# Optimization experiments

Hardware: AMD Instinct MI355X
Metric: run time of the kernel (lower is better)

The kernel has to match this reference:

```python
import jax, jax.numpy as jnp
import numpy as np

# model dims (DeepSeekV2-Lite-like, reduced expert count)
H = 2048      # hidden_dim
NH = 16       # num_heads
NOPE = 128    # qk_nope_head_dim
ROPE = 64     # qk_rope_head_dim (interleaved rotary)
VD = 128      # v_head_dim
QL = 1536     # q_lora_rank
KVL = 512     # kv_lora_rank
E = 8         # num routed experts
TOPK = 2      # num_experts_per_token
MI = 512      # moe_intermediate_dim
SH_I = 2 * MI # num_shared_experts * moe_intermediate_dim
B = 1
S = 2048
T = B * S
EPS = 1e-6
MOE_SCALE = 1.0  # gating_scaling_factor


def setup_inputs() -> dict:
    key = jax.random.key(0)
    ks = jax.random.split(key, 16)
    def w(k, shape):
        return jax.random.normal(k, shape, dtype=jnp.float32) * 0.02
    # interleaved rotary tables: one angle per (even,odd) pair
    half = ROPE // 2
    pos = jnp.arange(S, dtype=jnp.float32)
    inv_freq = 1.0 / (10000.0 ** (jnp.arange(half, dtype=jnp.float32) * 2.0 / ROPE))
    ang = pos[:, None] * inv_freq[None, :]              # [S, half]
    sin = jnp.tile(jnp.sin(ang), (B, 1))                # [T, half]
    cos = jnp.tile(jnp.cos(ang), (B, 1))
    return {
        "x": jax.random.normal(ks[0], (T, H), jnp.float32),
        "skip": jax.random.normal(ks[1], (T, H), jnp.float32),
        "rotary_sin": sin,
        "rotary_cos": cos,
        "ln1_w": jnp.ones((H,), jnp.float32),
        "ln2_w": jnp.ones((H,), jnp.float32),
        "w_qa": w(ks[2], (QL, H)),
        "qa_norm_w": jnp.ones((QL,), jnp.float32),
        "w_qb": w(ks[3], (NH * (NOPE + ROPE), QL)),
        "w_kva": w(ks[4], (KVL + ROPE, H)),
        "kva_norm_w": jnp.ones((KVL,), jnp.float32),
        "w_kb": w(ks[5], (NH * NOPE, KVL)),
        "w_vb": w(ks[6], (NH * VD, KVL)),
        "w_o": w(ks[7], (H, NH * VD)),
        "gate_w": w(ks[8], (E, H)),
        "moe_up_w": w(ks[9], (E, 2 * MI, H)),
        "moe_down_w": w(ks[10], (E, H, MI)),
        "shared_up_w": w(ks[11], (2 * SH_I, H)),
        "shared_down_w": w(ks[12], (H, SH_I)),
        "batch": B,
    }


def _rms(v, w):
    return v * jax.lax.rsqrt(jnp.mean(v * v, axis=-1, keepdims=True) + EPS) * w


def _rope_interleaved(v, sin, cos):
    # v: [T, nh, ROPE]; sin/cos: [T, ROPE//2]; rotate (even, odd) pairs
    x1, x2 = v[..., 0::2], v[..., 1::2]
    s, c = sin[:, None, :], cos[:, None, :]
    o1 = x1 * c - x2 * s
    o2 = x1 * s + x2 * c
    return jnp.stack([o1, o2], axis=-1).reshape(v.shape)


def reference(x, skip, rotary_sin, rotary_cos, ln1_w, ln2_w, w_qa, qa_norm_w,
              w_qb, w_kva, kva_norm_w, w_kb, w_vb, w_o, gate_w,
              moe_up_w, moe_down_w, shared_up_w, shared_down_w, batch):
    Tt = x.shape[0]
    Sq = Tt // batch
    # SkipRMSNorm #1
    x1 = x + skip
    n1 = _rms(x1, ln1_w)
    # ---- MLA attention (prefill path, decoding_batches=0) ----
    qa = _rms(n1 @ w_qa.T, qa_norm_w)                               # [T, QL]
    q = (qa @ w_qb.T).reshape(Tt, NH, NOPE + ROPE)
    q_nope, q_pe = q[..., :NOPE], q[..., NOPE:]
    q_pe = _rope_interleaved(q_pe, rotary_sin, rotary_cos)
    kv = n1 @ w_kva.T                                               # [T, KVL+ROPE]
    ckv = _rms(kv[:, :KVL], kva_norm_w)
    k_pe = _rope_interleaved(kv[:, KVL:][:, None, :], rotary_sin, rotary_cos)  # [T,1,ROPE]
    k_nope = (ckv @ w_kb.T).reshape(Tt, NH, NOPE)
    v = (ckv @ w_vb.T).reshape(Tt, NH, VD)
    qf = jnp.concatenate([q_nope, q_pe], -1).reshape(batch, Sq, NH, NOPE + ROPE)
    kf = jnp.concatenate([k_nope, jnp.broadcast_to(k_pe, (Tt, NH, ROPE))], -1)
    kf = kf.reshape(batch, Sq, NH, NOPE + ROPE)
    vf = v.reshape(batch, Sq, NH, VD)
    scale = 1.0 / np.sqrt(NOPE + ROPE)
    scores = jnp.einsum('bqhd,bkhd->bhqk', qf, kf) * scale
    causal = jnp.tril(jnp.ones((Sq, Sq), bool))
    scores = jnp.where(causal[None, None], scores, jnp.float32(-1e30))
    p = jax.nn.softmax(scores, axis=-1)
    o = jnp.einsum('bhqk,bkhd->bqhd', p, vf).reshape(Tt, NH * VD)
    attn = o @ w_o.T
    # SkipRMSNorm #2
    x2 = x1 + attn
    n2 = _rms(x2, ln2_w)
    # ---- MoE FFN: softmax gate, greedy top-k, normalized probs ----
    probs = jax.nn.softmax(n2 @ gate_w.T, axis=-1)                  # [T, E]
    tv, ti = jax.lax.top_k(probs, TOPK)
    tv = tv / jnp.sum(tv, axis=-1, keepdims=True) * MOE_SCALE
    routed = jnp.zeros_like(n2)
    for e in range(E):  # fixed small expert count; masked dense dispatch
        we = jnp.sum(tv * (ti == e), axis=-1)                       # [T]
        h = n2 @ moe_up_w[e].T                                      # [T, 2*MI]
        h = jax.nn.silu(h[:, :MI]) * h[:, MI:]
        routed = routed + we[:, None] * (h @ moe_down_w[e].T)
    # shared experts (dense swiglu MLP)
    hs = n2 @ shared_up_w.T
    hs = jax.nn.silu(hs[:, :SH_I]) * hs[:, SH_I:]
    ffn = routed + hs @ shared_down_w.T
    return (x2, ffn)
```

## Files before the change

kernel.cpp:

```cpp
#include <hip/hip_runtime.h>
#include <hip/hip_bf16.h>

#define H 2048
#define NH 16
#define NOPE 128
#define ROPE_D 64
#define DQK 192
#define VD 128
#define QL 1536
#define KVL 512
#define NE 8
#define MI_D 512
#define SHI 1024
#define EPS 1e-6f
#define MAXA 5120

typedef unsigned short bfu;
typedef short bf16x8 __attribute__((ext_vector_type(8)));
typedef float f32x4 __attribute__((ext_vector_type(4)));

#define MFMA16(a, b, c) __builtin_amdgcn_mfma_f32_16x16x32_bf16(a, b, c, 0, 0, 0)

#define BAR_PLAIN()   asm volatile("s_barrier" ::: "memory")
#define BAR_LGKM0()   asm volatile("s_waitcnt lgkmcnt(0)\n\ts_barrier" ::: "memory")
#define BAR_VM4()     asm volatile("s_waitcnt vmcnt(4)\n\ts_barrier" ::: "memory")
#define BAR_VM0()     asm volatile("s_waitcnt vmcnt(0)\n\ts_barrier" ::: "memory")

__device__ __forceinline__ float bf2f(bfu u) {
    union { unsigned int i; float f; } w; w.i = ((unsigned int)u) << 16; return w.f;
}
__device__ __forceinline__ bfu f2bf(float f) {
    union { float f; unsigned int i; } u; u.f = f;
    return (bfu)((u.i + 0x7fffu + ((u.i >> 16) & 1u)) >> 16);
}

__device__ __forceinline__ void async16(const bfu* g, bfu* l) {
    __builtin_amdgcn_global_load_lds((const __attribute__((address_space(1))) void*)g,
                                     (__attribute__((address_space(3))) void*)l, 16, 0, 0);
}

__device__ __forceinline__ float blk_sum(float v) {
    __shared__ float sb[4];
    for (int o = 32; o > 0; o >>= 1) v += __shfl_down(v, o, 64);
    int lane = threadIdx.x & 63, w = threadIdx.x >> 6;
    __syncthreads();
    if (lane == 0) sb[w] = v;
    __syncthreads();
    return sb[0] + sb[1] + sb[2] + sb[3];
}

struct GemmSeg {
    const bfu* A; const bfu* B; void* C; void* C2;
    const int* aidx; const int* eid;
    long bstride;
    int N, K, ldm3, mode, nx, ntiles;
};

__device__ __forceinline__ void gemm_body(const bfu* __restrict__ A, const bfu* __restrict__ B,
                                          void* __restrict__ Cv, void* __restrict__ Cv2,
                                          int N, int K, int ldm3, int mode,
                                          const int* __restrict__ aidx,
                                          const int* __restrict__ eid, long bstride,
                                          int bx, int by,
                                          bfu* sAb, bfu* sBb) {
    bfu (*sA)[128 * 32] = (bfu (*)[128 * 32])sAb;
    bfu (*sB)[128 * 32] = (bfu (*)[128 * 32])sBb;
    const int tid = threadIdx.x;
    const int lane = tid & 63, w = tid >> 6;
    const int quad = lane >> 4, li = lane & 15;
    const int m0 = by * 128, n0 = bx * 128;
    const bfu* Bp = B + (eid ? (size_t)eid[by] * bstride : 0);

    const int l4 = lane >> 2;
    const int lg = lane & 3;
    const int kc = lg ^ ((lane >> 3) & 3);
    int r0 = m0 + w * 32 + l4, r1 = r0 + 16;
    if (aidx) { r0 = aidx[r0]; r1 = aidx[r1]; }
    const bfu* gA0 = A + (size_t)r0 * K + kc * 8;
    const bfu* gA1 = A + (size_t)r1 * K + kc * 8;
    const bfu* gB0 = Bp + (size_t)(n0 + w * 32 + l4) * K + kc * 8;
    const bfu* gB1 = gB0 + (size_t)16 * K;
    const int oA0 = (w * 32) * 32, oA1 = (w * 32 + 16) * 32;

    const int wm = (w >> 1) * 64, wn = (w & 1) * 64;
    const int fg = (quad ^ ((li >> 1) & 3)) * 8;
    int oa[4], ob[4];
#pragma unroll
    for (int t4 = 0; t4 < 4; ++t4) {
        oa[t4] = (wm + t4 * 16 + li) * 32 + fg;
        ob[t4] = (wn + t4 * 16 + li) * 32 + fg;
    }
    f32x4 acc[4][4];
#pragma unroll
    for (int i = 0; i < 4; ++i)
#pragma unroll
        for (int j = 0; j < 4; ++j) acc[i][j] = (f32x4){0.f, 0.f, 0.f, 0.f};

    const int nb = K / 32;
    async16(gA0, &sA[0][oA0]); async16(gA1, &sA[0][oA1]);
    async16(gB0, &sB[0][oA0]); async16(gB1, &sB[0][oA1]);
    async16(gA0 + 32, &sA[1][oA0]); async16(gA1 + 32, &sA[1][oA1]);
    async16(gB0 + 32, &sB[1][oA0]); async16(gB1 + 32, &sB[1][oA1]);

    int cur = 0;
    for (int it = 0; it < nb; ++it) {
        if (it < nb - 1) { BAR_VM4(); } else { BAR_VM0(); }
        bf16x8 av[4], bv[4];
#pragma unroll
        for (int t4 = 0; t4 < 4; ++t4) av[t4] = *(const bf16x8*)&sA[cur][oa[t4]];
#pragma unroll
        for (int t4 = 0; t4 < 4; ++t4) bv[t4] = *(const bf16x8*)&sB[cur][ob[t4]];
        if (it + 2 < nb) {
            const int k1 = (it + 2) * 32;
            int nxt = cur + 2; if (nxt >= 3) nxt -= 3;
            async16(gA0 + k1, &sA[nxt][oA0]); async16(gA1 + k1, &sA[nxt][oA1]);
            async16(gB0 + k1, &sB[nxt][oA0]); async16(gB1 + k1, &sB[nxt][oA1]);
        }
#pragma unroll
        for (int mt = 0; mt < 4; ++mt)
#pragma unroll
            for (int nt = 0; nt < 4; ++nt)
                acc[mt][nt] = MFMA16(av[mt], bv[nt], acc[mt][nt]);
        if (++cur >= 3) cur = 0;
    }

#pragma unroll
    for (int mt = 0; mt < 4; ++mt)
#pragma unroll
        for (int nt = 0; nt < 4; ++nt) {
            int row = m0 + wm + mt * 16 + quad * 4;
            int col = n0 + wn + nt * 16 + li;
            if (mode == 0) {
                float* C = (float*)Cv;
#pragma unroll
                for (int r = 0; r < 4; ++r) C[(size_t)(row + r) * N + col] = acc[mt][nt][r];
            } else if (mode == 1) {
                bfu* C = (bfu*)Cv;
#pragma unroll
                for (int r = 0; r < 4; ++r) C[(size_t)(row + r) * N + col] = f2bf(acc[mt][nt][r]);
            } else {
                if (n0 < 2048) {
                    bfu* C = (bfu*)Cv;
#pragma unroll
                    for (int r = 0; r < 4; ++r) C[(size_t)(row + r) * 2048 + col] = f2bf(acc[mt][nt][r]);
                } else {
                    bfu* C2 = (bfu*)Cv2;
                    ushort4 u;
                    u.x = f2bf(acc[mt][nt][0]); u.y = f2bf(acc[mt][nt][1]);
                    u.z = f2bf(acc[mt][nt][2]); u.w = f2bf(acc[mt][nt][3]);
                    *(ushort4*)(C2 + (size_t)(col - 2048) * ldm3 + row) = u;
                }
            }
        }
}

__global__ __launch_bounds__(256) void gemm_multi(GemmSeg s0, GemmSeg s1) {
    __shared__ bfu sA[3][128 * 32];
    __shared__ bfu sB[3][128 * 32];
    int b = blockIdx.x;
    if (b < s0.ntiles) {
        gemm_body(s0.A, s0.B, s0.C, s0.C2, s0.N, s0.K, s0.ldm3, s0.mode,
                  s0.aidx, s0.eid, s0.bstride, b % s0.nx, b / s0.nx, &sA[0][0], &sB[0][0]);
    } else {
        int lb = b - s0.ntiles;
        gemm_body(s1.A, s1.B, s1.C, s1.C2, s1.N, s1.K, s1.ldm3, s1.mode,
                  s1.aidx, s1.eid, s1.bstride, lb % s1.nx, lb / s1.nx, &sA[0][0], &sB[0][0]);
    }
}

struct CastArgs {
    const float* s[10];
    bfu* d[10];
    unsigned start[11];
    int pad[10];
};
__global__ __launch_bounds__(256) void k_cast_all(CastArgs a) {
    unsigned g = blockIdx.x * 256 + threadIdx.x;
    if (g >= a.start[10]) return;
    int id = 0;
#pragma unroll
    for (int i = 1; i < 10; ++i) if (g >= a.start[i]) id = i;
    size_t i16 = (size_t)(g - a.start[id]) * 16;
    ushort4 u[4] = {};
    if (!a.pad[id] || (i16 >> 11) < 576) {
        const float* s = a.s[id];
#pragma unroll
        for (int j = 0; j < 4; ++j) {
            float4 x = *(const float4*)(s + i16 + j * 4);
            u[j].x = f2bf(x.x); u[j].y = f2bf(x.y); u[j].z = f2bf(x.z); u[j].w = f2bf(x.w);
        }
    }
    bfu* d = a.d[id];
#pragma unroll
    for (int j = 0; j < 4; ++j) *(ushort4*)(d + i16 + j * 4) = u[j];
}

__global__ __launch_bounds__(256) void k_add_rms(const float* __restrict__ x, const float* __restrict__ skip,
                                                 const float* __restrict__ w,
                                                 float* __restrict__ x1, bfu* __restrict__ n1b) {
    int t = blockIdx.x;
    size_t base = (size_t)t * H;
    float loc[8]; float ss = 0.f;
#pragma unroll
    for (int i = 0; i < 8; ++i) {
        int c = threadIdx.x + i * 256;
        float v = x[base + c] + skip[base + c];
        loc[i] = v; ss += v * v;
        x1[base + c] = v;
    }
    float tot = blk_sum(ss);
    float r = rsqrtf(tot / (float)H + EPS);
#pragma unroll
    for (int i = 0; i < 8; ++i) {
        int c = threadIdx.x + i * 256;
        n1b[base + c] = f2bf(loc[i] * r * w[c]);
    }
}

__global__ __launch_bounds__(256) void k_qkv_post(const bfu* __restrict__ qkv,
                                                  const float* __restrict__ qa_nw,
                                                  const float* __restrict__ kva_nw,
                                                  const float* __restrict__ sin_, const float* __restrict__ cos_,
                                                  bfu* __restrict__ qab, bfu* __restrict__ ckv,
                                                  bfu* __restrict__ kpe) {
    int t = blockIdx.x;
    const bfu* row = qkv + (size_t)t * 2176;
    float qa[6]; float ss1 = 0.f;
#pragma unroll
    for (int i = 0; i < 6; ++i) {
        float v = bf2f(row[threadIdx.x + i * 256]); qa[i] = v; ss1 += v * v;
    }
    float v0 = bf2f(row[1536 + threadIdx.x]), v1 = bf2f(row[1792 + threadIdx.x]);
    float s1 = blk_sum(ss1);
    float s2 = blk_sum(v0 * v0 + v1 * v1);
    float r1 = rsqrtf(s1 / (float)QL + EPS);
    float r2 = rsqrtf(s2 / 512.f + EPS);
#pragma unroll
    for (int i = 0; i < 6; ++i) {
        int c = threadIdx.x + i * 256;
        qab[(size_t)t * QL + c] = f2bf(qa[i] * r1 * qa_nw[c]);
    }
    ckv[(size_t)t * 512 + threadIdx.x]       = f2bf(v0 * r2 * kva_nw[threadIdx.x]);
    ckv[(size_t)t * 512 + threadIdx.x + 256] = f2bf(v1 * r2 * kva_nw[threadIdx.x + 256]);
    if (threadIdx.x < 32) {
        int p = threadIdx.x;
        float x1v = bf2f(row[2048 + 2 * p]), x2v = bf2f(row[2048 + 2 * p + 1]);
        float s = sin_[t * 32 + p], c = cos_[t * 32 + p];
        kpe[(size_t)t * 64 + 2 * p]     = f2bf(x1v * c - x2v * s);
        kpe[(size_t)t * 64 + 2 * p + 1] = f2bf(x1v * s + x2v * c);
    }
}

__global__ __launch_bounds__(256) void k_flash_mfma(const bfu* __restrict__ qb,
                                                    const bfu* __restrict__ kn,
                                                    const bfu* __restrict__ kpe,
                                                    const bfu* __restrict__ vt,
                                                    bfu* __restrict__ O,
                                                    const float* __restrict__ rsin,
                                                    const float* __restrict__ rcos, int T) {
    __shared__ bfu Ks[64 * 200];
    __shared__ bfu VtL[2][128 * 32];
    __shared__ bfu P[64 * 72];
    const int tid = threadIdx.x;
    const int lane = tid & 63, w = tid >> 6;
    const int quad = lane >> 4, li = lane & 15;
    const int q0 = ((int)gridDim.x - 1 - (int)blockIdx.x) * 64;
    const int h = blockIdx.y;
    const float scale = 0.07216878364870322f;

    bf16x8 qf[6];
    {
        int qrow = q0 + w * 16 + li;
        const bfu* qp = qb + ((size_t)qrow * NH + h) * DQK;
#pragma unroll
        for (int s6 = 0; s6 < 6; ++s6) {
            bf16x8 v = *(const bf16x8*)(qp + s6 * 32 + quad * 8);
            if (s6 >= 4) {
                int pb = (s6 - 4) * 16 + quad * 4;
#pragma unroll
                for (int j = 0; j < 4; ++j) {
                    float x1 = bf2f((bfu)v[2 * j]), x2 = bf2f((bfu)v[2 * j + 1]);
                    float s = rsin[qrow * 32 + pb + j], c = rcos[qrow * 32 + pb + j];
                    v[2 * j]     = (short)f2bf(x1 * c - x2 * s);
                    v[2 * j + 1] = (short)f2bf(x1 * s + x2 * c);
                }
            }
            qf[s6] = v;
        }
    }
    f32x4 accO[8];
#pragma unroll
    for (int i = 0; i < 8; ++i) accO[i] = (f32x4){0.f, 0.f, 0.f, 0.f};
    float lrow[4] = {0.f, 0.f, 0.f, 0.f};

    int kr[6], kg[6];
#pragma unroll
    for (int it = 0; it < 6; ++it) { int G = tid + it * 256; kr[it] = G / 24; kg[it] = G % 24; }
    int vn[4], vgl[4], vkc[4];
#pragma unroll
    for (int it = 0; it < 4; ++it) {
        int idx = tid + it * 256; vn[it] = idx >> 3; vgl[it] = idx & 7;
        vkc[it] = (vgl[it] & 4) | ((vgl[it] & 3) ^ ((vn[it] >> 1) & 3));
    }
    bf16x8 kreg[6], vreg[4];
#pragma unroll
    for (int it = 0; it < 6; ++it)
        kreg[it] = (kg[it] < 16) ? *(const bf16x8*)(kn + (size_t)kr[it] * (NH * 128) + h * 128 + kg[it] * 8)
                                 : *(const bf16x8*)(kpe + (size_t)kr[it] * 64 + (kg[it] - 16) * 8);
#pragma unroll
    for (int it = 0; it < 4; ++it)
        vreg[it] = *(const bf16x8*)(vt + (size_t)(h * 128 + vn[it]) * T + vkc[it] * 8);

    const int fgv = (quad ^ ((li >> 1) & 3)) * 8;
    const int kend = q0 + 64;
    for (int k0 = 0; k0 < kend; k0 += 64) {
        BAR_PLAIN();
#pragma unroll
        for (int it = 0; it < 6; ++it) *(bf16x8*)(Ks + kr[it] * 200 + kg[it] * 8) = kreg[it];
#pragma unroll
        for (int it = 0; it < 4; ++it)
            *(bf16x8*)(VtL[vgl[it] >> 2] + vn[it] * 32 + (vgl[it] & 3) * 8) = vreg[it];
        if (k0 + 64 < kend) {
            int k1 = k0 + 64;
#pragma unroll
            for (int it = 0; it < 6; ++it)
                kreg[it] = (kg[it] < 16) ? *(const bf16x8*)(kn + (size_t)(k1 + kr[it]) * (NH * 128) + h * 128 + kg[it] * 8)
                                         : *(const bf16x8*)(kpe + (size_t)(k1 + kr[it]) * 64 + (kg[it] - 16) * 8);
#pragma unroll
            for (int it = 0; it < 4; ++it)
                vreg[it] = *(const bf16x8*)(vt + (size_t)(h * 128 + vn[it]) * T + k1 + vkc[it] * 8);
        }
        BAR_LGKM0();
        f32x4 s[4];
#pragma unroll
        for (int ct = 0; ct < 4; ++ct) {
            f32x4 a = (f32x4){0.f, 0.f, 0.f, 0.f};
#pragma unroll
            for (int s6 = 0; s6 < 6; ++s6) {
                bf16x8 kf = *(const bf16x8*)(Ks + (ct * 16 + li) * 200 + s6 * 32 + quad * 8);
                a = MFMA16(qf[s6], kf, a);
            }
            s[ct] = a;
        }
#pragma unroll
        for (int ct = 0; ct < 4; ++ct)
#pragma unroll
            for (int r = 0; r < 4; ++r) {
                int row = q0 + w * 16 + quad * 4 + r;
                float p = (k0 + ct * 16 + li <= row) ? __expf(s[ct][r] * scale) : 0.f;
                s[ct][r] = p;
                lrow[r] += p;
            }
#pragma unroll
        for (int ct = 0; ct < 4; ++ct)
#pragma unroll
            for (int r = 0; r < 4; ++r)
                P[(w * 16 + quad * 4 + r) * 72 + ct * 16 + li] = f2bf(s[ct][r]);
        bf16x8 pf[2];
#pragma unroll
        for (int ks = 0; ks < 2; ++ks)
            pf[ks] = *(const bf16x8*)(P + (w * 16 + li) * 72 + ks * 32 + quad * 8);
#pragma unroll
        for (int v8 = 0; v8 < 8; ++v8)
#pragma unroll
            for (int ks = 0; ks < 2; ++ks) {
                bf16x8 vf = *(const bf16x8*)(VtL[ks] + (v8 * 16 + li) * 32 + fgv);
                accO[v8] = MFMA16(pf[ks], vf, accO[v8]);
            }
    }
#pragma unroll
    for (int r = 0; r < 4; ++r) {
        float l = lrow[r];
        l += __shfl_xor(l, 1); l += __shfl_xor(l, 2);
        l += __shfl_xor(l, 4); l += __shfl_xor(l, 8);
        lrow[r] = 1.0f / l;
    }
#pragma unroll
    for (int v8 = 0; v8 < 8; ++v8)
#pragma unroll
        for (int r = 0; r < 4; ++r) {
            float val = accO[v8][r] * lrow[r];
            O[(size_t)(q0 + w * 16 + quad * 4 + r) * (NH * 128) + h * 128 + v8 * 16 + li] = f2bf(val);
        }
}

__global__ __launch_bounds__(256) void k_x2_n2(const float* __restrict__ x1, const bfu* __restrict__ attn,
                                               const float* __restrict__ ln2w, float* __restrict__ outx2,
                                               bfu* __restrict__ n2b, const float* __restrict__ gw,
                                               int* __restrict__ eidx, float* __restrict__ wts,
                                               int* __restrict__ cnt) {
    int t = blockIdx.x;
    size_t base = (size_t)t * H;
    float loc[8]; float ss = 0.f;
#pragma unroll
    for (int i = 0; i < 8; ++i) {
        int c = threadIdx.x + i * 256;
        float vv = x1[base + c] + bf2f(attn[base + c]);
        loc[i] = vv; ss += vv * vv;
        outx2[base + c] = vv;
    }
    float tot = blk_sum(ss);
    float r = rsqrtf(tot / (float)H + EPS);
    float pe[NE] = {0.f, 0.f, 0.f, 0.f, 0.f, 0.f, 0.f, 0.f};
#pragma unroll
    for (int i = 0; i < 8; ++i) {
        int c = threadIdx.x + i * 256;
        float nv = loc[i] * r * ln2w[c];
        n2b[base + c] = f2bf(nv);
#pragma unroll
        for (int e = 0; e < NE; ++e) pe[e] += nv * gw[e * H + c];
    }
    __shared__ float sred[4][NE];
    int lane = threadIdx.x & 63, wv = threadIdx.x >> 6;
#pragma unroll
    for (int e = 0; e < NE; ++e) {
        float v = pe[e];
        for (int o = 32; o > 0; o >>= 1) v += __shfl_down(v, o, 64);
        if (lane == 0) sred[wv][e] = v;
    }
    __syncthreads();
    if (threadIdx.x == 0) {
        float logits[NE];
        float m = -1e30f;
        for (int e = 0; e < NE; ++e) {
            logits[e] = sred[0][e] + sred[1][e] + sred[2][e] + sred[3][e];
            m = fmaxf(m, logits[e]);
        }
        float p[NE];
        for (int e = 0; e < NE; ++e) p[e] = __expf(logits[e] - m);
        int i1 = 0;
        for (int e = 1; e < NE; ++e) if (p[e] > p[i1]) i1 = e;
        int i2 = -1;
        for (int e = 0; e < NE; ++e) if (e != i1 && (i2 < 0 || p[e] > p[i2])) i2 = e;
        float denom = p[i1] + p[i2];
        eidx[t * 2] = i1; eidx[t * 2 + 1] = i2;
        wts[t * 2] = p[i1] / denom; wts[t * 2 + 1] = p[i2] / denom;
        atomicAdd(&cnt[i1], 1); atomicAdd(&cnt[i2], 1);
    }
}

__global__ __launch_bounds__(256) void k_moe_init(int* __restrict__ cnt, int* __restrict__ slot,
                                                  int* __restrict__ eid, int* __restrict__ idx,
                                                  float* __restrict__ aw) {
    int tid = threadIdx.x;
    if (tid < NE) { cnt[tid] = 0; slot[tid] = 0; }
    if (tid < 40) eid[tid] = 0;
    for (int i = tid; i < MAXA; i += 256) { idx[i] = 0; aw[i] = 0.f; }
}

__global__ __launch_bounds__(64) void k_moe_scan(const int* __restrict__ cnt, int* __restrict__ base,
                                                 int* __restrict__ eid) {
    if (threadIdx.x == 0) {
        int off = 0;
        for (int e = 0; e < NE; ++e) {
            base[e] = off;
            int nb = (cnt[e] + 127) >> 7;
            for (int j = 0; j < nb; ++j) eid[(off >> 7) + j] = e;
            off += nb << 7;
        }
    }
}

__global__ __launch_bounds__(256) void k_moe_scatter(const int* __restrict__ eidx, const float* __restrict__ wts,
                                                     const int* __restrict__ base, int* __restrict__ slot,
                                                     int* __restrict__ idx, float* __restrict__ aw,
                                                     int* __restrict__ posmap) {
    int t = blockIdx.x * 256 + threadIdx.x;
#pragma unroll
    for (int j = 0; j < 2; ++j) {
        int e = eidx[t * 2 + j];
        int p = base[e] + atomicAdd(&slot[e], 1);
        idx[p] = t; aw[p] = wts[t * 2 + j]; posmap[t * 2 + j] = p;
    }
}

__global__ __launch_bounds__(256) void k_silu_both(const bfu* __restrict__ hsh, bfu* __restrict__ gsh,
                                                   const bfu* __restrict__ hsp, const float* __restrict__ aw,
                                                   bfu* __restrict__ gsp, int T) {
    int b = blockIdx.x;
    if (b < T) {
        const bfu* row = hsh + (size_t)b * 2048;
        bfu* grow = gsh + (size_t)b * 1024;
#pragma unroll
        for (int j = 0; j < 4; ++j) {
            int i = threadIdx.x + j * 256;
            float a = bf2f(row[i]), bb = bf2f(row[1024 + i]);
            grow[i] = f2bf(a / (1.0f + __expf(-a)) * bb);
        }
    } else {
        int row = b - T;
        float we = aw[row];
        const bfu* hr = hsp + (size_t)row * 1024;
        bfu* gr = gsp + (size_t)row * 512;
#pragma unroll
        for (int j = 0; j < 2; ++j) {
            int i = threadIdx.x + j * 256;
            float a = bf2f(hr[i]), bb = bf2f(hr[512 + i]);
            gr[i] = f2bf(we * a / (1.0f + __expf(-a)) * bb);
        }
    }
}

__global__ __launch_bounds__(256) void k_ffn_out(const float* __restrict__ routed, const bfu* __restrict__ dsp,
                                                 const int* __restrict__ posmap, float* __restrict__ out,
                                                 size_t TH) {
    int t = blockIdx.x;
    int p1 = posmap[t * 2], p2 = posmap[t * 2 + 1];
    const bfu* d1 = dsp + (size_t)p1 * H;
    const bfu* d2 = dsp + (size_t)p2 * H;
#pragma unroll
    for (int j = 0; j < 8; ++j) {
        int c = threadIdx.x + j * 256;
        out[TH + (size_t)t * H + c] = routed[(size_t)t * H + c] + bf2f(d1[c]) + bf2f(d2[c]);
    }
}

static inline GemmSeg mk_seg(const bfu* A, const bfu* B, void* C, void* C2,
                             const int* aidx, const int* eid, long bstride,
                             int N, int K, int ldm3, int mode, int nx, int ny) {
    GemmSeg s;
    s.A = A; s.B = B; s.C = C; s.C2 = C2; s.aidx = aidx; s.eid = eid; s.bstride = bstride;
    s.N = N; s.K = K; s.ldm3 = ldm3; s.mode = mode; s.nx = nx; s.ntiles = nx * ny;
    return s;
}

extern "C" void kernel_launch(void* const* d_in, const int* in_sizes, int n_in,
                              void* d_out, int out_size, void* d_ws, size_t ws_size,
                              hipStream_t stream) {
    const float* x      = (const float*)d_in[0];
    const float* skip   = (const float*)d_in[1];
    const float* rsin   = (const float*)d_in[2];
    const float* rcos   = (const float*)d_in[3];
    const float* ln1w   = (const float*)d_in[4];
    const float* ln2w   = (const float*)d_in[5];
    const float* w_qa   = (const float*)d_in[6];
    const float* qa_nw  = (const float*)d_in[7];
    const float* w_qb   = (const float*)d_in[8];
    const float* w_kva  = (const float*)d_in[9];
    const float* kva_nw = (const float*)d_in[10];
    const float* w_kb   = (const float*)d_in[11];
    const float* w_vb   = (const float*)d_in[12];
    const float* w_o    = (const float*)d_in[13];
    const float* gate_w = (const float*)d_in[14];
    const float* mup    = (const float*)d_in[15];
    const float* mdown  = (const float*)d_in[16];
    const float* shup   = (const float*)d_in[17];
    const float* shdown = (const float*)d_in[18];

    const int T = in_sizes[0] / H;

    bfu* WB = (bfu*)d_ws;
    bfu* wqkv_b  = WB + 0;
    bfu* wkbv_b  = WB + 4456448;
    bfu* wqb_b   = WB + 6553600;
    bfu* wo_b    = WB + 11272192;
    bfu* mup_b   = WB + 15466496;
    bfu* mdown_b = WB + 32243712;
    bfu* shup_b  = WB + 40632320;
    bfu* shdn_b  = WB + 44826624;
    const size_t WBYTES = 93847552;

    char* AB = (char*)d_ws + WBYTES;
    float* x1f    = (float*)(AB + 0);
    float* routed = (float*)(AB + 0);
    bfu*   n1b    = (bfu*)(AB + 16777216);
    bfu*   qkvb   = (bfu*)(AB + 25165824);
    bfu*   knb    = (bfu*)(AB + 25165824);
    bfu*   hsp    = (bfu*)(AB + 25165824);
    bfu*   qab    = (bfu*)(AB + 35651584);
    bfu*   gsp    = (bfu*)(AB + 35651584);
    bfu*   qbb    = (bfu*)(AB + 41943040);
    bfu*   attnb  = (bfu*)(AB + 41943040);
    bfu*   ckvb   = (bfu*)(AB + 54525952);
    bfu*   kpeb   = (bfu*)(AB + 56623104);
    char*  G      = AB + 56885248;
    int*   eidx   = (int*)(G);
    float* wts    = (float*)(G + 16384);
    int*   posmap = (int*)(G + 32768);
    int*   midx   = (int*)(G + 49152);
    float* maw    = (float*)(G + 69632);
    int*   mcnt   = (int*)(G + 90112);
    int*   mbase  = (int*)(G + 90112 + 64);
    int*   mslot  = (int*)(G + 90112 + 128);
    int*   meid   = (int*)(G + 90112 + 192);
    bfu*   ob     = (bfu*)(AB + 57016320);
    bfu*   gsb    = (bfu*)(AB + 57016320);
    bfu*   vtb    = (bfu*)(AB + 65404928);
    bfu*   hsb    = (bfu*)(AB + 65404928);
    bfu*   dsp    = (bfu*)(AB + 65404928);
    const size_t REQ = WBYTES + 86376448;
    if (ws_size < REQ) return;

    {
        CastArgs ca;
        const float* ss[10] = {w_qa, w_kva, w_kb, w_vb, w_qb, w_o, mup, mdown, shup, shdown};
        bfu* dd[10] = {wqkv_b, wqkv_b + 3145728, wkbv_b, wkbv_b + 1048576, wqb_b,
                       wo_b, mup_b, mdown_b, shup_b, shdn_b};
        unsigned n16[10] = {196608, 81920, 65536, 65536, 294912, 262144, 1048576, 524288, 262144, 131072};
        unsigned acc = 0;
        for (int i = 0; i < 10; ++i) { ca.s[i] = ss[i]; ca.d[i] = dd[i]; ca.start[i] = acc; acc += n16[i]; ca.pad[i] = (i == 1); }
        ca.start[10] = acc;
        k_cast_all<<<(acc + 255) / 256, 256, 0, stream>>>(ca);
    }

    k_add_rms<<<T, 256, 0, stream>>>(x, skip, ln1w, x1f, n1b);
    {
        GemmSeg s = mk_seg(n1b, wqkv_b, qkvb, nullptr, nullptr, nullptr, 0, 2176, H, 0, 1, 2176 / 128, T / 128);
        gemm_multi<<<s.ntiles, 256, 0, stream>>>(s, s);
    }
    k_qkv_post<<<T, 256, 0, stream>>>(qkvb, qa_nw, kva_nw, rsin, rcos, qab, ckvb, kpeb);
    {
        GemmSeg sq = mk_seg(qab, wqb_b, qbb, nullptr, nullptr, nullptr, 0, NH * DQK, QL, 0, 1, (NH * DQK) / 128, T / 128);
        GemmSeg sk = mk_seg(ckvb, wkbv_b, knb, vtb, nullptr, nullptr, 0, 4096, KVL, T, 4, 4096 / 128, T / 128);
        gemm_multi<<<sq.ntiles + sk.ntiles, 256, 0, stream>>>(sq, sk);
    }
    k_flash_mfma<<<dim3(T / 64, NH), 256, 0, stream>>>(qbb, knb, kpeb, vtb, ob, rsin, rcos, T);
    {
        GemmSeg s = mk_seg(ob, wo_b, attnb, nullptr, nullptr, nullptr, 0, H, NH * VD, 0, 1, H / 128, T / 128);
        gemm_multi<<<s.ntiles, 256, 0, stream>>>(s, s);
    }
    k_moe_init<<<1, 256, 0, stream>>>(mcnt, mslot, meid, midx, maw);
    k_x2_n2<<<T, 256, 0, stream>>>(x1f, attnb, ln2w, (float*)d_out, n1b, gate_w, eidx, wts, mcnt);
    k_moe_scan<<<1, 64, 0, stream>>>(mcnt, mbase, meid);
    k_moe_scatter<<<T / 256, 256, 0, stream>>>(eidx, wts, mbase, mslot, midx, maw, posmap);
    {
        GemmSeg ssh = mk_seg(n1b, shup_b, hsb, nullptr, nullptr, nullptr, 0, 2048, H, 0, 1, 2048 / 128, T / 128);
        GemmSeg smo = mk_seg(n1b, mup_b, hsp, nullptr, midx, meid, (long)1024 * H, 1024, H, 0, 1, 1024 / 128, MAXA / 128);
        gemm_multi<<<ssh.ntiles + smo.ntiles, 256, 0, stream>>>(ssh, smo);
    }
    k_silu_both<<<T + MAXA, 256, 0, stream>>>(hsb, gsb, hsp, maw, gsp, T);
    {
        GemmSeg ssd = mk_seg(gsb, shdn_b, routed, nullptr, nullptr, nullptr, 0, H, SHI, 0, 0, H / 128, T / 128);
        GemmSeg smd = mk_seg(gsp, mdown_b, dsp, nullptr, nullptr, meid, (long)H * MI_D, H, MI_D, 0, 1, H / 128, MAXA / 128);
        gemm_multi<<<ssd.ntiles + smd.ntiles, 256, 0, stream>>>(ssd, smd);
    }
    k_ffn_out<<<T, 256, 0, stream>>>(routed, dsp, posmap, (float*)d_out, (size_t)T * H);
}
```

Measured before the change: 638.0 us.

## Split weight casts across GEMM launches to overlap conversion with compute

The single up-front fp32-to-bf16 weight cast kernel is removed. Its work is split into four groups, and each group is appended as extra blocks to an earlier gemm_multi launch, so every weight is converted just before the GEMM that needs it. This lets the memory-bound cast run alongside compute-bound GEMM tiles. In exchange, the gemm_multi kernel now carries a large CastArgs struct and a third branch, and the cast blocks share the LDS allocation size of the GEMM blocks, which may limit how many of them stay resident at once.

```diff
diff --git a/kernel.cpp b/kernel.cpp
--- a/kernel.cpp
+++ b/kernel.cpp
@@ -54,6 +54,13 @@
     const int* aidx; const int* eid;
     long bstride;
     int N, K, ldm3, mode, nx, ntiles;
+};
+
+struct CastArgs {
+    const float* s[10];
+    bfu* d[10];
+    unsigned start[11];
+    int pad[10];
 };
 
 __device__ __forceinline__ void gemm_body(const bfu* __restrict__ A, const bfu* __restrict__ B,
@@ -154,45 +161,37 @@
         }
 }
 
-__global__ __launch_bounds__(256) void gemm_multi(GemmSeg s0, GemmSeg s1) {
+__global__ __launch_bounds__(256) void gemm_multi(GemmSeg s0, GemmSeg s1, CastArgs ca) {
     __shared__ bfu sA[3][128 * 32];
     __shared__ bfu sB[3][128 * 32];
     int b = blockIdx.x;
     if (b < s0.ntiles) {
         gemm_body(s0.A, s0.B, s0.C, s0.C2, s0.N, s0.K, s0.ldm3, s0.mode,
                   s0.aidx, s0.eid, s0.bstride, b % s0.nx, b / s0.nx, &sA[0][0], &sB[0][0]);
-    } else {
+    } else if (b < s0.ntiles + s1.ntiles) {
         int lb = b - s0.ntiles;
         gemm_body(s1.A, s1.B, s1.C, s1.C2, s1.N, s1.K, s1.ldm3, s1.mode,
                   s1.aidx, s1.eid, s1.bstride, lb % s1.nx, lb / s1.nx, &sA[0][0], &sB[0][0]);
-    }
-}
-
-struct CastArgs {
-    const float* s[10];
-    bfu* d[10];
-    unsigned start[11];
-    int pad[10];
-};
-__global__ __launch_bounds__(256) void k_cast_all(CastArgs a) {
-    unsigned g = blockIdx.x * 256 + threadIdx.x;
-    if (g >= a.start[10]) return;
-    int id = 0;
-#pragma unroll
-    for (int i = 1; i < 10; ++i) if (g >= a.start[i]) id = i;
-    size_t i16 = (size_t)(g - a.start[id]) * 16;
-    ushort4 u[4] = {};
-    if (!a.pad[id] || (i16 >> 11) < 576) {
-        const float* s = a.s[id];
-#pragma unroll
-        for (int j = 0; j < 4; ++j) {
-            float4 x = *(const float4*)(s + i16 + j * 4);
-            u[j].x = f2bf(x.x); u[j].y = f2bf(x.y); u[j].z = f2bf(x.z); u[j].w = f2bf(x.w);
-        }
-    }
-    bfu* d = a.d[id];
-#pragma unroll
-    for (int j = 0; j < 4; ++j) *(ushort4*)(d + i16 + j * 4) = u[j];
+    } else {
+        unsigned g = (unsigned)(b - s0.ntiles - s1.ntiles) * 256 + threadIdx.x;
+        if (g >= ca.start[10]) return;
+        int id = 0;
+#pragma unroll
+        for (int i = 1; i < 10; ++i) if (g >= ca.start[i]) id = i;
+        size_t i16 = (size_t)(g - ca.start[id]) * 16;
+        ushort4 u[4] = {};
+        if (!ca.pad[id] || (i16 >> 11) < 576) {
+            const float* s = ca.s[id];
+#pragma unroll
+            for (int j = 0; j < 4; ++j) {
+                float4 xv = *(const float4*)(s + i16 + j * 4);
+                u[j].x = f2bf(xv.x); u[j].y = f2bf(xv.y); u[j].z = f2bf(xv.z); u[j].w = f2bf(xv.w);
+            }
+        }
+        bfu* d = ca.d[id];
+#pragma unroll
+        for (int j = 0; j < 4; ++j) *(ushort4*)(d + i16 + j * 4) = u[j];
+    }
 }
 
 __global__ __launch_bounds__(256) void k_add_rms(const float* __restrict__ x, const float* __restrict__ skip,
@@ -522,6 +521,21 @@
     s.A = A; s.B = B; s.C = C; s.C2 = C2; s.aidx = aidx; s.eid = eid; s.bstride = bstride;
     s.N = N; s.K = K; s.ldm3 = ldm3; s.mode = mode; s.nx = nx; s.ntiles = nx * ny;
     return s;
+}
+
+static inline CastArgs mk_cast(int n, const float* const ss[], bfu* const dd[],
+                               const unsigned nn[], const int pp[]) {
+    CastArgs ca;
+    unsigned acc = 0;
+    for (int i = 0; i < n; ++i) {
+        ca.s[i] = ss[i]; ca.d[i] = dd[i]; ca.pad[i] = pp[i];
+        ca.start[i] = acc; acc += nn[i];
+    }
+    for (int i = n; i < 10; ++i) {
+        ca.s[i] = ss[n - 1]; ca.d[i] = dd[n - 1]; ca.pad[i] = 0; ca.start[i] = acc;
+    }
+    ca.start[10] = acc;
+    return ca;
 }
 
 extern "C" void kernel_launch(void* const* d_in, const int* in_sizes, int n_in,
@@ -591,33 +605,54 @@
     const size_t REQ = WBYTES + 86376448;
     if (ws_size < REQ) return;
 
-    {
-        CastArgs ca;
-        const float* ss[10] = {w_qa, w_kva, w_kb, w_vb, w_qb, w_o, mup, mdown, shup, shdown};
-        bfu* dd[10] = {wqkv_b, wqkv_b + 3145728, wkbv_b, wkbv_b + 1048576, wqb_b,
-                       wo_b, mup_b, mdown_b, shup_b, shdn_b};
-        unsigned n16[10] = {196608, 81920, 65536, 65536, 294912, 262144, 1048576, 524288, 262144, 131072};
-        unsigned acc = 0;
-        for (int i = 0; i < 10; ++i) { ca.s[i] = ss[i]; ca.d[i] = dd[i]; ca.start[i] = acc; acc += n16[i]; ca.pad[i] = (i == 1); }
-        ca.start[10] = acc;
-        k_cast_all<<<(acc + 255) / 256, 256, 0, stream>>>(ca);
-    }
-
+    GemmSeg z; z.A = nullptr; z.B = nullptr; z.C = nullptr; z.C2 = nullptr;
+    z.aidx = nullptr; z.eid = nullptr; z.bstride = 0;
+    z.N = 0; z.K = 32; z.ldm3 = 0; z.mode = 1; z.nx = 1; z.ntiles = 0;
+
+    const float* c0s[2] = {w_qa, w_kva};
+    bfu*         c0d[2] = {wqkv_b, wqkv_b + 3145728};
+    unsigned     c0n[2] = {196608, 81920};
+    int          c0p[2] = {0, 1};
+    CastArgs ca0 = mk_cast(2, c0s, c0d, c0n, c0p);
+
+    const float* cQs[3] = {w_qb, w_kb, w_vb};
+    bfu*         cQd[3] = {wqb_b, wkbv_b, wkbv_b + 1048576};
+    unsigned     cQn[3] = {294912, 65536, 65536};
+    int          cQp[3] = {0, 0, 0};
+    CastArgs caQ = mk_cast(3, cQs, cQd, cQn, cQp);
+
+    const float* cBs[2] = {w_o, mup};
+    bfu*         cBd[2] = {wo_b, mup_b};
+    unsigned     cBn[2] = {262144, 1048576};
+    int          cBp[2] = {0, 0};
+    CastArgs caB = mk_cast(2, cBs, cBd, cBn, cBp);
+
+    const float* cWs[3] = {shup, mdown, shdown};
+    bfu*         cWd[3] = {shup_b, mdown_b, shdn_b};
+    unsigned     cWn[3] = {262144, 524288, 131072};
+    int          cWp[3] = {0, 0, 0};
+    CastArgs caW = mk_cast(3, cWs, cWd, cWn, cWp);
+
+    const float* cEs[1] = {w_qa}; bfu* cEd[1] = {wqkv_b};
+    unsigned cEn[1] = {0}; int cEp[1] = {0};
+    CastArgs caE = mk_cast(1, cEs, cEd, cEn, cEp);
+
+    gemm_multi<<<1088, 256, 0, stream>>>(z, z, ca0);
     k_add_rms<<<T, 256, 0, stream>>>(x, skip, ln1w, x1f, n1b);
     {
         GemmSeg s = mk_seg(n1b, wqkv_b, qkvb, nullptr, nullptr, nullptr, 0, 2176, H, 0, 1, 2176 / 128, T / 128);
-        gemm_multi<<<s.ntiles, 256, 0, stream>>>(s, s);
+        gemm_multi<<<s.ntiles + 1664, 256, 0, stream>>>(s, z, caQ);
     }
     k_qkv_post<<<T, 256, 0, stream>>>(qkvb, qa_nw, kva_nw, rsin, rcos, qab, ckvb, kpeb);
     {
         GemmSeg sq = mk_seg(qab, wqb_b, qbb, nullptr, nullptr, nullptr, 0, NH * DQK, QL, 0, 1, (NH * DQK) / 128, T / 128);
         GemmSeg sk = mk_seg(ckvb, wkbv_b, knb, vtb, nullptr, nullptr, 0, 4096, KVL, T, 4, 4096 / 128, T / 128);
-        gemm_multi<<<sq.ntiles + sk.ntiles, 256, 0, stream>>>(sq, sk);
+        gemm_multi<<<sq.ntiles + sk.ntiles + 5120, 256, 0, stream>>>(sq, sk, caB);
     }
     k_flash_mfma<<<dim3(T / 64, NH), 256, 0, stream>>>(qbb, knb, kpeb, vtb, ob, rsin, rcos, T);
     {
         GemmSeg s = mk_seg(ob, wo_b, attnb, nullptr, nullptr, nullptr, 0, H, NH * VD, 0, 1, H / 128, T / 128);
-        gemm_multi<<<s.ntiles, 256, 0, stream>>>(s, s);
+        gemm_multi<<<s.ntiles + 3584, 256, 0, stream>>>(s, z, caW);
     }
     k_moe_init<<<1, 256, 0, stream>>>(mcnt, mslot, meid, midx, maw);
     k_x2_n2<<<T, 256, 0, stream>>>(x1f, attnb, ln2w, (float*)d_out, n1b, gate_w, eidx, wts, mcnt);
@@ -626,13 +661,13 @@
     {
         GemmSeg ssh = mk_seg(n1b, shup_b, hsb, nullptr, nullptr, nullptr, 0, 2048, H, 0, 1, 2048 / 128, T / 128);
         GemmSeg smo = mk_seg(n1b, mup_b, hsp, nullptr, midx, meid, (long)1024 * H, 1024, H, 0, 1, 1024 / 128, MAXA / 128);
-        gemm_multi<<<ssh.ntiles + smo.ntiles, 256, 0, stream>>>(ssh, smo);
+        gemm_multi<<<ssh.ntiles + smo.ntiles, 256, 0, stream>>>(ssh, smo, caE);
     }
     k_silu_both<<<T + MAXA, 256, 0, stream>>>(hsb, gsb, hsp, maw, gsp, T);
     {
         GemmSeg ssd = mk_seg(gsb, shdn_b, routed, nullptr, nullptr, nullptr, 0, H, SHI, 0, 0, H / 128, T / 128);
         GemmSeg smd = mk_seg(gsp, mdown_b, dsp, nullptr, nullptr, meid, (long)H * MI_D, H, MI_D, 0, 1, H / 128, MAXA / 128);
-        gemm_multi<<<ssd.ntiles + smd.ntiles, 256, 0, stream>>>(ssd, smd);
+        gemm_multi<<<ssd.ntiles + smd.ntiles, 256, 0, stream>>>(ssd, smd, caE);
     }
     k_ffn_out<<<T, 256, 0, stream>>>(routed, dsp, posmap, (float*)d_out, (size_t)T * H);
 }
```

After: 610.0 us. -4.4%, faster.
